# Optimization experiments

Hardware: AMD Instinct MI355X
Metric: run time of the kernel (lower is better)

The kernel has to match this reference:

```python
import jax, jax.numpy as jnp
import numpy as np

N, E, DIN, HID, DOUT = 50000, 800000, 128, 128, 64
NEG_SLOPE = 0.2


def setup_inputs() -> dict:
    key = jax.random.key(0)
    ks = jax.random.split(key, 16)
    x = jax.random.normal(ks[0], (N, DIN), dtype=jnp.float32)
    edge_index = jax.random.randint(ks[1], (2, E), 0, N, dtype=jnp.int64)

    def lin(k, fan_in, fan_out):
        kw, kb = jax.random.split(k)
        s = 1.0 / np.sqrt(fan_in)
        W = jax.random.uniform(kw, (fan_in, fan_out), jnp.float32, -s, s)
        b = jax.random.uniform(kb, (fan_out,), jnp.float32, -s, s)
        return W, b

    Wl, bl = lin(ks[2], DIN, DIN)   # GATv2 lin_l
    Wr, br = lin(ks[3], DIN, DIN)   # GATv2 lin_r
    att = jax.random.uniform(ks[4], (DIN,), jnp.float32, -1.0 / np.sqrt(DIN), 1.0 / np.sqrt(DIN))
    bg = jnp.zeros((DIN,), jnp.float32)  # GAT output bias
    W1, b1 = lin(ks[5], DIN, HID)   # ChebConv K=1 -> plain linear
    W2, b2 = lin(ks[6], HID, HID)
    W3, b3 = lin(ks[7], HID, DOUT)
    return {"x": x, "edge_index": edge_index, "Wl": Wl, "bl": bl, "Wr": Wr,
            "br": br, "att": att, "bg": bg, "W1": W1, "b1": b1,
            "W2": W2, "b2": b2, "W3": W3, "b3": b3}


def reference(x, edge_index, Wl, bl, Wr, br, att, bg, W1, b1, W2, b2, W3, b3):
    n = x.shape[0]
    # GATv2Conv adds self loops by default
    loop = jnp.arange(n, dtype=edge_index.dtype)
    src = jnp.concatenate([edge_index[0], loop])  # source j
    dst = jnp.concatenate([edge_index[1], loop])  # target i

    xl = x @ Wl + bl  # [N, DIN]
    xr = x @ Wr + br  # [N, DIN]

    # GATv2 edge scores: leaky_relu(x_l[j] + x_r[i]) . att
    e = jax.nn.leaky_relu(xl[src] + xr[dst], NEG_SLOPE)  # [E+N, DIN]
    a = e @ att                                          # [E+N]

    # softmax over incoming edges of each destination node
    amax = jax.ops.segment_max(a, dst, num_segments=n)
    ea = jnp.exp(a - amax[dst])
    denom = jax.ops.segment_sum(ea, dst, num_segments=n)
    alpha = ea / denom[dst]                              # [E+N]

    # aggregate messages alpha * x_l[j] at destinations
    h = jax.ops.segment_sum(alpha[:, None] * xl[src], dst, num_segments=n) + bg

    # ChebConv with K=1 reduces to a linear layer (T_0(L) = I)
    h = jax.nn.relu(h @ W1 + b1)
    h = jax.nn.relu(h @ W2 + b2)
    # dropout_rate = 0.0 -> identity
    return h @ W3 + b3
```

## Files before the change

### kernel.cpp

```cpp
#include <hip/hip_runtime.h>
#include <hip/hip_bf16.h>

#define DIN 128
#define NEG_SLOPE 0.2f
#define PTILE 1024
#define FCAP 8192
#define CVT_BLKS 289

typedef __attribute__((ext_vector_type(8))) short bf16x8;
typedef __attribute__((ext_vector_type(8))) unsigned short u16x8;
typedef __attribute__((ext_vector_type(4))) float f32x4;
typedef __attribute__((ext_vector_type(2))) float f32x2;
typedef __attribute__((ext_vector_type(4))) unsigned int u32x4;

__device__ __forceinline__ ushort f2bf(float f) {
  unsigned u = __float_as_uint(f);
  u += 0x7FFFu + ((u >> 16) & 1u);
  return (ushort)(u >> 16);
}
__device__ __forceinline__ f32x2 bfpair(unsigned u) {
  f32x2 r;
  r.x = __uint_as_float(u << 16);
  r.y = __uint_as_float(u & 0xFFFF0000u);
  return r;
}

template <int CTRL>
__device__ __forceinline__ float dppadd(float x) {
  int v = __builtin_amdgcn_update_dpp(0, __float_as_int(x), CTRL, 0xf, 0xf, true);
  return x + __int_as_float(v);
}
__device__ __forceinline__ float red16(float t) {
  t = dppadd<0xB1>(t);
  t = dppadd<0x4E>(t);
  t = dppadd<0x141>(t);
  t = dppadd<0x140>(t);
  return t;
}

__global__ __launch_bounds__(256) void cvt_hist_kernel(
    const float* __restrict__ Wl, const float* __restrict__ Wr,
    const float* __restrict__ W1, const float* __restrict__ W2,
    const float* __restrict__ W3,
    ushort* __restrict__ WlT, ushort* __restrict__ WrT,
    ushort* __restrict__ W1T, ushort* __restrict__ W2T,
    ushort* __restrict__ W3T,
    const int* __restrict__ ei, int* __restrict__ ghist, int E) {
  if (blockIdx.x < CVT_BLKS) {
    int i = blockIdx.x * 256 + threadIdx.x;
    if (i < 16384) {
      int k = i >> 7, c = i & 127; WlT[c * 128 + k] = f2bf(Wl[i]);
    } else if (i < 32768) {
      int j = i - 16384; int k = j >> 7, c = j & 127; WrT[c * 128 + k] = f2bf(Wr[j]);
    } else if (i < 49152) {
      int j = i - 32768; int k = j >> 7, c = j & 127; W1T[c * 128 + k] = f2bf(W1[j]);
    } else if (i < 65536) {
      int j = i - 49152; int k = j >> 7, c = j & 127; W2T[c * 128 + k] = f2bf(W2[j]);
    } else if (i < 73728) {
      int j = i - 65536; int k = j >> 6, c = j & 63; W3T[c * 128 + k] = f2bf(W3[j]);
    }
  } else {
    __shared__ int h[256];
    h[threadIdx.x] = 0;
    __syncthreads();
    int tile = blockIdx.x - CVT_BLKS;
    for (int e = tile * PTILE + threadIdx.x;
         e < min(E, (tile + 1) * PTILE); e += 256)
      atomicAdd(&h[ei[E + e] >> 8], 1);
    __syncthreads();
    if (h[threadIdx.x] > 0) atomicAdd(&ghist[threadIdx.x], h[threadIdx.x]);
  }
}

__global__ __launch_bounds__(256) void lin_partition_kernel(
    const float* __restrict__ x,
    const ushort* __restrict__ WlT, const float* __restrict__ bl,
    const ushort* __restrict__ WrT, const float* __restrict__ br,
    ushort* __restrict__ xl, ushort* __restrict__ xr, int n, int nblk_lin,
    const int* __restrict__ ei, unsigned* __restrict__ part,
    const int* __restrict__ ghist, int* __restrict__ cursor0, int E) {
  if ((int)blockIdx.x < nblk_lin) {
    const int tid = threadIdx.x;
    const int wv = tid >> 6, lane = tid & 63;
    const int m = lane & 15, quad = lane >> 4;
    const int colbase = (wv & 1) * 64;
    const int nodew = blockIdx.x * 32 + (wv >> 1) * 16;
    int arow = nodew + m; if (arow >= n) arow = n - 1;
    f32x4 accl[4], accr[4];
#pragma unroll
    for (int nt = 0; nt < 4; nt++) { accl[nt] = (f32x4){0,0,0,0}; accr[nt] = (f32x4){0,0,0,0}; }
#pragma unroll
    for (int kk = 0; kk < 4; kk++) {
      int k0 = kk * 32 + quad * 8;
      const float4* xp = (const float4*)(x + (long)arow * 128 + k0);
      float4 x0 = xp[0], x1 = xp[1];
      bf16x8 af;
      af[0] = (short)f2bf(x0.x); af[1] = (short)f2bf(x0.y);
      af[2] = (short)f2bf(x0.z); af[3] = (short)f2bf(x0.w);
      af[4] = (short)f2bf(x1.x); af[5] = (short)f2bf(x1.y);
      af[6] = (short)f2bf(x1.z); af[7] = (short)f2bf(x1.w);
#pragma unroll
      for (int nt = 0; nt < 4; nt++) {
        int brow = colbase + nt * 16 + m;
        bf16x8 bl8 = *(const bf16x8*)(WlT + brow * 128 + k0);
        bf16x8 br8 = *(const bf16x8*)(WrT + brow * 128 + k0);
        accl[nt] = __builtin_amdgcn_mfma_f32_16x16x32_bf16(af, bl8, accl[nt], 0, 0, 0);
        accr[nt] = __builtin_amdgcn_mfma_f32_16x16x32_bf16(af, br8, accr[nt], 0, 0, 0);
      }
    }
#pragma unroll
    for (int nt = 0; nt < 4; nt++) {
      int col = colbase + nt * 16 + m;
      float vbl = bl[col], vbr = br[col];
#pragma unroll
      for (int r = 0; r < 4; r++) {
        int node = nodew + quad * 4 + r;
        if (node < n) {
          xl[(long)node * 128 + col] = f2bf(accl[nt][r] + vbl);
          xr[(long)node * 128 + col] = f2bf(accr[nt][r] + vbr);
        }
      }
    }
  } else {
    __shared__ int hist[256], pref[256], sexcl[256], curs[256], gbase[256],
                   gsc[256];
    const int tid = threadIdx.x;
    const int gv0 = ghist[tid];
    gsc[tid] = gv0;
    hist[tid] = 0;
    __syncthreads();
    __shared__ unsigned buf[PTILE];
    const int tile0 = ((int)blockIdx.x - nblk_lin) * PTILE;
    const int tcount = min(PTILE, E - tile0);
    unsigned pk[PTILE / 256];
    int cnt = 0;
    for (int i = tid; i < tcount; i += 256) {
      int e = tile0 + i;
      int s = ei[e], d = ei[E + e];
      unsigned p = ((unsigned)d << 16) | (unsigned)s;
      pk[cnt++] = p;
      atomicAdd(&hist[d >> 8], 1);
    }
    __syncthreads();
    int v = hist[tid];
    pref[tid] = v;
    __syncthreads();
    for (int d = 1; d < 256; d <<= 1) {
      int t1 = (tid >= d) ? pref[tid - d] : 0;
      int t2 = (tid >= d) ? gsc[tid - d] : 0;
      __syncthreads();
      pref[tid] += t1;
      gsc[tid] += t2;
      __syncthreads();
    }
    int exc = pref[tid] - v;
    sexcl[tid] = exc;
    curs[tid] = exc;
    gbase[tid] = (gsc[tid] - gv0) + ((v > 0) ? atomicAdd(&cursor0[tid], v) : 0);
    __syncthreads();
    for (int j = 0; j < cnt; j++) {
      int b = pk[j] >> 24;
      int pos = atomicAdd(&curs[b], 1);
      buf[pos] = pk[j];
    }
    __syncthreads();
    for (int i = tid; i < tcount; i += 256) {
      unsigned p = buf[i];
      int b = p >> 24;
      part[gbase[b] + (i - sexcl[b])] = p;
    }
  }
}

__global__ __launch_bounds__(512) void fine_kernel(
    const unsigned* __restrict__ part, const int* __restrict__ ghist,
    int* __restrict__ offsets, ushort* __restrict__ ssrc,
    int N, int E, int nbuck) {
  __shared__ int hist[256], pref[256], curs[256], gsc[256];
  __shared__ unsigned buf[FCAP], buf2[FCAP];
  const int tid = threadIdx.x;
  const int b = blockIdx.x;
  if (tid < 256) {
    gsc[tid] = ghist[tid];
    hist[tid] = 0;
  }
  __syncthreads();
  for (int d = 1; d < 256; d <<= 1) {
    int t = (tid >= d && tid < 256) ? gsc[tid - d] : 0;
    __syncthreads();
    if (tid < 256) gsc[tid] += t;
    __syncthreads();
  }
  const int seg0 = (b == 0) ? 0 : gsc[b - 1];
  const int len = min(gsc[b] - seg0, FCAP);
  for (int i = tid; i < len; i += 512) {
    unsigned p = part[seg0 + i];
    buf[i] = p;
    atomicAdd(&hist[(p >> 16) & 255], 1);
  }
  __syncthreads();
  int v = (tid < 256) ? hist[tid] : 0;
  if (tid < 256) pref[tid] = v;
  __syncthreads();
  for (int d = 1; d < 256; d <<= 1) {
    int t = (tid >= d && tid < 256) ? pref[tid - d] : 0;
    __syncthreads();
    if (tid < 256) pref[tid] += t;
    __syncthreads();
  }
  if (tid < 256) {
    int exc = pref[tid] - v;
    curs[tid] = exc;
    int node = b * 256 + tid;
    if (node < N) offsets[node] = seg0 + exc;
  }
  if (b == nbuck - 1 && tid == 0) offsets[N] = E;
  __syncthreads();
  for (int i = tid; i < len; i += 512) {
    unsigned p = buf[i];
    int pos = atomicAdd(&curs[(p >> 16) & 255], 1);
    buf2[pos] = p;
  }
  __syncthreads();
  for (int i = tid; i < len; i += 512)
    ssrc[seg0 + i] = (ushort)(buf2[i] & 0xFFFFu);
}

#define LDSP 136
__global__ __launch_bounds__(256) void node_mlp_kernel(
    const ushort* __restrict__ xl, const ushort* __restrict__ xr,
    const float* __restrict__ att, const float* __restrict__ bg,
    const int* __restrict__ offsets, const ushort* __restrict__ ssrc,
    const ushort* __restrict__ W1T, const float* __restrict__ b1,
    const ushort* __restrict__ W2T, const float* __restrict__ b2,
    const ushort* __restrict__ W3T, const float* __restrict__ b3,
    float* __restrict__ out, int n) {
  __shared__ ushort hst[32][LDSP];
  __shared__ ushort act[32][LDSP];
  const int tid = threadIdx.x;
  const int wv = tid >> 6, lane = tid & 63;
  {
    const int eg = lane >> 4, sl = lane & 15;
    const ushort* __restrict__ xls = xl + sl * 8;
    f32x2 a06[4], a04[4], gvb[4];
    {
      const float4* ap = (const float4*)(att + sl * 8);
      float4 a0 = ap[0], a1 = ap[1];
      f32x2 av[4] = {{a0.x, a0.y}, {a0.z, a0.w}, {a1.x, a1.y}, {a1.z, a1.w}};
#pragma unroll
      for (int jp = 0; jp < 4; jp++) {
        a06[jp] = 0.6f * av[jp];
        a04[jp] = 0.4f * av[jp];
      }
      const float4* bp = (const float4*)(bg + sl * 8);
      float4 g0 = bp[0], g1 = bp[1];
      gvb[0] = (f32x2){g0.x, g0.y}; gvb[1] = (f32x2){g0.z, g0.w};
      gvb[2] = (f32x2){g1.x, g1.y}; gvb[3] = (f32x2){g1.z, g1.w};
    }
    for (int nn = 0; nn < 8; nn++) {
      const int node = (int)blockIdx.x * 32 + wv * 8 + nn;
      if (node >= n) continue;
      const int beg = offsets[node];
      const int end = offsets[node + 1];
      const int last = end - 1;
      int ia0 = beg + 2 * eg;
      int sa  = (int)ssrc[min(ia0, last)];
      int sb  = (int)ssrc[min(ia0 + 1, last)];
      int sa2 = (int)ssrc[min(ia0 + 8, last)];
      int sb2 = (int)ssrc[min(ia0 + 9, last)];
      u32x4 uva = *(const u32x4*)(xls + (long)sa * 128);
      u32x4 uvb = *(const u32x4*)(xls + (long)sb * 128);
      f32x2 r2[4], acc2[4];
      u32x4 rv = *(const u32x4*)(xr + (long)node * 128 + sl * 8);
      u32x4 lv = *(const u32x4*)(xls + (long)node * 128);
      float denom;
      {
        f32x2 t1 = {0.f, 0.f}, t2 = {0.f, 0.f};
        f32x2 l2[4];
#pragma unroll
        for (int jp = 0; jp < 4; jp++) {
          r2[jp] = bfpair(rv[jp]);
          l2[jp] = bfpair(lv[jp]);
          f32x2 v = l2[jp] + r2[jp];
          t1 += a06[jp] * v;
          t2 += a04[jp] * __builtin_elementwise_abs(v);
        }
        float t = red16(t1.x + t1.y + t2.x + t2.y);
        float es = __expf(t);
        denom = (eg == 0) ? es : 0.f;
#pragma unroll
        for (int jp = 0; jp < 4; jp++)
          acc2[jp] = (eg == 0) ? es * l2[jp] : (f32x2){0.f, 0.f};
      }
      for (int p = beg; p < end; p += 8) {
        u32x4 ca = uva, cb = uvb;
        int ia = p + 2 * eg;
        bool cva = ia < end, cvb = ia + 1 < end;
        uva = *(const u32x4*)(xls + (long)sa2 * 128);
        uvb = *(const u32x4*)(xls + (long)sb2 * 128);
        int ian = p + 16 + 2 * eg;
        sa2 = (int)ssrc[min(ian, last)];
        sb2 = (int)ssrc[min(ian + 1, last)];
        f32x2 ua2[4], ub2[4];
        f32x2 ta1 = {0.f, 0.f}, ta2 = {0.f, 0.f};
        f32x2 tb1 = {0.f, 0.f}, tb2 = {0.f, 0.f};
#pragma unroll
        for (int jp = 0; jp < 4; jp++) {
          ua2[jp] = bfpair(ca[jp]);
          ub2[jp] = bfpair(cb[jp]);
          f32x2 va2 = ua2[jp] + r2[jp];
          f32x2 vb2 = ub2[jp] + r2[jp];
          ta1 += a06[jp] * va2;
          ta2 += a04[jp] * __builtin_elementwise_abs(va2);
          tb1 += a06[jp] * vb2;
          tb2 += a04[jp] * __builtin_elementwise_abs(vb2);
        }
        float ta = red16(ta1.x + ta1.y + ta2.x + ta2.y);
        float tb = red16(tb1.x + tb1.y + tb2.x + tb2.y);
        float ea = cva ? __expf(ta) : 0.f;
        float eb = cvb ? __expf(tb) : 0.f;
        denom += ea + eb;
#pragma unroll
        for (int jp = 0; jp < 4; jp++)
          acc2[jp] += ea * ua2[jp] + eb * ub2[jp];
      }
#pragma unroll
      for (int jp = 0; jp < 4; jp++) {
        acc2[jp].x += __shfl_xor(acc2[jp].x, 16);
        acc2[jp].y += __shfl_xor(acc2[jp].y, 16);
        acc2[jp].x += __shfl_xor(acc2[jp].x, 32);
        acc2[jp].y += __shfl_xor(acc2[jp].y, 32);
      }
      denom += __shfl_xor(denom, 16);
      denom += __shfl_xor(denom, 32);
      if (eg == 0) {
        float inv = 1.0f / denom;
        u16x8 o;
#pragma unroll
        for (int jp = 0; jp < 4; jp++) {
          f32x2 hv = acc2[jp] * inv + gvb[jp];
          o[2 * jp]     = f2bf(hv.x);
          o[2 * jp + 1] = f2bf(hv.y);
        }
        *(u16x8*)(&hst[wv * 8 + nn][sl * 8]) = o;
      }
    }
  }
  __syncthreads();
  const int m = lane & 15, quad = lane >> 4;
  const int half = wv & 1, ng = wv >> 1;
  const int colbase = half * 64;
  const int nodew = (int)blockIdx.x * 32 + ng * 16;
  f32x4 acc[4];
#pragma unroll
  for (int nt = 0; nt < 4; nt++) acc[nt] = (f32x4){0,0,0,0};
#pragma unroll
  for (int kk = 0; kk < 4; kk++) {
    int k0 = kk * 32 + quad * 8;
    bf16x8 af = *(const bf16x8*)(&hst[ng * 16 + m][k0]);
#pragma unroll
    for (int nt = 0; nt < 4; nt++) {
      bf16x8 b8 = *(const bf16x8*)(W1T + (colbase + nt * 16 + m) * 128 + k0);
      acc[nt] = __builtin_amdgcn_mfma_f32_16x16x32_bf16(af, b8, acc[nt], 0, 0, 0);
    }
  }
#pragma unroll
  for (int nt = 0; nt < 4; nt++) {
    int col = colbase + nt * 16 + m;
    float b = b1[col];
#pragma unroll
    for (int r = 0; r < 4; r++)
      act[ng * 16 + quad * 4 + r][col] = f2bf(fmaxf(acc[nt][r] + b, 0.f));
  }
  __syncthreads();
#pragma unroll
  for (int nt = 0; nt < 4; nt++) acc[nt] = (f32x4){0,0,0,0};
#pragma unroll
  for (int kk = 0; kk < 4; kk++) {
    int k0 = kk * 32 + quad * 8;
    bf16x8 af = *(const bf16x8*)(&act[ng * 16 + m][k0]);
#pragma unroll
    for (int nt = 0; nt < 4; nt++) {
      bf16x8 b8 = *(const bf16x8*)(W2T + (colbase + nt * 16 + m) * 128 + k0);
      acc[nt] = __builtin_amdgcn_mfma_f32_16x16x32_bf16(af, b8, acc[nt], 0, 0, 0);
    }
  }
  __syncthreads();
#pragma unroll
  for (int nt = 0; nt < 4; nt++) {
    int col = colbase + nt * 16 + m;
    float b = b2[col];
#pragma unroll
    for (int r = 0; r < 4; r++)
      act[ng * 16 + quad * 4 + r][col] = f2bf(fmaxf(acc[nt][r] + b, 0.f));
  }
  __syncthreads();
  f32x4 acc3[2];
#pragma unroll
  for (int nt = 0; nt < 2; nt++) acc3[nt] = (f32x4){0,0,0,0};
#pragma unroll
  for (int kk = 0; kk < 4; kk++) {
    int k0 = kk * 32 + quad * 8;
    bf16x8 af = *(const bf16x8*)(&act[ng * 16 + m][k0]);
#pragma unroll
    for (int nt = 0; nt < 2; nt++) {
      bf16x8 b8 = *(const bf16x8*)(W3T + (half * 32 + nt * 16 + m) * 128 + k0);
      acc3[nt] = __builtin_amdgcn_mfma_f32_16x16x32_bf16(af, b8, acc3[nt], 0, 0, 0);
    }
  }
#pragma unroll
  for (int nt = 0; nt < 2; nt++) {
    int col = half * 32 + nt * 16 + m;
    float b = b3[col];
#pragma unroll
    for (int r = 0; r < 4; r++) {
      int node = nodew + quad * 4 + r;
      if (node < n) out[(long)node * 64 + col] = acc3[nt][r] + b;
    }
  }
}

extern "C" void kernel_launch(void* const* d_in, const int* in_sizes, int n_in,
                              void* d_out, int out_size, void* d_ws, size_t ws_size,
                              hipStream_t stream) {
  const float* x   = (const float*)d_in[0];
  const int*   ei  = (const int*)d_in[1];
  const float* Wl  = (const float*)d_in[2];
  const float* bl  = (const float*)d_in[3];
  const float* Wr  = (const float*)d_in[4];
  const float* br  = (const float*)d_in[5];
  const float* att = (const float*)d_in[6];
  const float* bg  = (const float*)d_in[7];
  const float* W1  = (const float*)d_in[8];
  const float* b1  = (const float*)d_in[9];
  const float* W2  = (const float*)d_in[10];
  const float* b2  = (const float*)d_in[11];
  const float* W3  = (const float*)d_in[12];
  const float* b3  = (const float*)d_in[13];
  float* out = (float*)d_out;

  const int N = in_sizes[0] / DIN;
  const int E = in_sizes[1] / 2;
  const int nbuck = (N + 255) >> 8;

  char* ws = (char*)d_ws;
  size_t off = 0;
  auto alloc = [&](size_t bytes) {
    void* p = ws + off;
    off += (bytes + 255) & ~(size_t)255;
    return p;
  };
  int* ghist     = (int*)alloc(256 * 4);
  int* cursor0   = (int*)alloc(256 * 4);
  int* offsets   = (int*)alloc(((size_t)N + 4) * 4);
  unsigned* part = (unsigned*)alloc((size_t)E * 4);
  ushort* ssrc   = (ushort*)alloc(((size_t)E + 16) * 2);
  ushort* xlb    = (ushort*)alloc((size_t)N * DIN * 2);
  ushort* xrb    = (ushort*)alloc((size_t)N * DIN * 2);
  ushort* WlT    = (ushort*)alloc(16384 * 2);
  ushort* WrT    = (ushort*)alloc(16384 * 2);
  ushort* W1T    = (ushort*)alloc(16384 * 2);
  ushort* W2T    = (ushort*)alloc(16384 * 2);
  ushort* W3T    = (ushort*)alloc(8192 * 2);
  (void)ws_size;

  hipMemsetAsync(ghist, 0, 512 * 4, stream);

  int ntile = (E + PTILE - 1) / PTILE;
  cvt_hist_kernel<<<CVT_BLKS + ntile, 256, 0, stream>>>(
      Wl, Wr, W1, W2, W3, WlT, WrT, W1T, W2T, W3T, ei, ghist, E);

  int nblk32 = (N + 31) / 32;
  lin_partition_kernel<<<nblk32 + ntile, 256, 0, stream>>>(
      x, WlT, bl, WrT, br, xlb, xrb, N, nblk32, ei, part, ghist, cursor0, E);

  fine_kernel<<<nbuck, 512, 0, stream>>>(part, ghist, offsets, ssrc, N, E, nbuck);

  node_mlp_kernel<<<nblk32, 256, 0, stream>>>(
      xlb, xrb, att, bg, offsets, ssrc,
      W1T, b1, W2T, b2, W3T, b3, out, N);
}
```

Before: 253.8 us.

## Split GAT aggregation from MLP and compute per-node degree histogram globally

The fused aggregation+MLP kernel, where each wave handled eight nodes in sequence, is split in two. A new aggregation kernel assigns one wave per node and writes h to a global bf16 buffer, and a separate MFMA kernel runs the three linear layers from that buffer. The fine sort kernel drops its LDS buffering and local histogram pass and instead uses a per-node in-degree histogram built with global atomics in the first kernel, scattering directly into ssrc. This aims to improve load balance and occupancy and removes the FCAP cap, at the cost of an extra launch, an h round trip through global memory, and 800k global atomics.

```diff
diff --git a/kernel.cpp b/kernel.cpp
--- a/kernel.cpp
+++ b/kernel.cpp
@@ -4,7 +4,6 @@
 #define DIN 128
 #define NEG_SLOPE 0.2f
 #define PTILE 1024
-#define FCAP 8192
 #define CVT_BLKS 289
 
 typedef __attribute__((ext_vector_type(8))) short bf16x8;
@@ -45,7 +44,8 @@
     ushort* __restrict__ WlT, ushort* __restrict__ WrT,
     ushort* __restrict__ W1T, ushort* __restrict__ W2T,
     ushort* __restrict__ W3T,
-    const int* __restrict__ ei, int* __restrict__ ghist, int E) {
+    const int* __restrict__ ei, int* __restrict__ ghist,
+    int* __restrict__ nhist, int E) {
   if (blockIdx.x < CVT_BLKS) {
     int i = blockIdx.x * 256 + threadIdx.x;
     if (i < 16384) {
@@ -65,8 +65,11 @@
     __syncthreads();
     int tile = blockIdx.x - CVT_BLKS;
     for (int e = tile * PTILE + threadIdx.x;
-         e < min(E, (tile + 1) * PTILE); e += 256)
-      atomicAdd(&h[ei[E + e] >> 8], 1);
+         e < min(E, (tile + 1) * PTILE); e += 256) {
+      int d = ei[E + e];
+      atomicAdd(&h[d >> 8], 1);
+      atomicAdd(&nhist[d], 1);
+    }
     __syncthreads();
     if (h[threadIdx.x] > 0) atomicAdd(&ghist[threadIdx.x], h[threadIdx.x]);
   }
@@ -174,190 +177,177 @@
 
 __global__ __launch_bounds__(512) void fine_kernel(
     const unsigned* __restrict__ part, const int* __restrict__ ghist,
+    const int* __restrict__ nhist,
     int* __restrict__ offsets, ushort* __restrict__ ssrc,
     int N, int E, int nbuck) {
-  __shared__ int hist[256], pref[256], curs[256], gsc[256];
-  __shared__ unsigned buf[FCAP], buf2[FCAP];
+  __shared__ int gsc[256], nsc[256], curs[256];
   const int tid = threadIdx.x;
   const int b = blockIdx.x;
+  int nv = 0;
   if (tid < 256) {
     gsc[tid] = ghist[tid];
-    hist[tid] = 0;
+    int node = b * 256 + tid;
+    nv = (node < N) ? nhist[node] : 0;
+    nsc[tid] = nv;
   }
   __syncthreads();
   for (int d = 1; d < 256; d <<= 1) {
-    int t = (tid >= d && tid < 256) ? gsc[tid - d] : 0;
-    __syncthreads();
-    if (tid < 256) gsc[tid] += t;
+    int t1 = (tid >= d && tid < 256) ? gsc[tid - d] : 0;
+    int t2 = (tid >= d && tid < 256) ? nsc[tid - d] : 0;
+    __syncthreads();
+    if (tid < 256) { gsc[tid] += t1; nsc[tid] += t2; }
     __syncthreads();
   }
   const int seg0 = (b == 0) ? 0 : gsc[b - 1];
-  const int len = min(gsc[b] - seg0, FCAP);
-  for (int i = tid; i < len; i += 512) {
-    unsigned p = part[seg0 + i];
-    buf[i] = p;
-    atomicAdd(&hist[(p >> 16) & 255], 1);
-  }
-  __syncthreads();
-  int v = (tid < 256) ? hist[tid] : 0;
-  if (tid < 256) pref[tid] = v;
-  __syncthreads();
-  for (int d = 1; d < 256; d <<= 1) {
-    int t = (tid >= d && tid < 256) ? pref[tid - d] : 0;
-    __syncthreads();
-    if (tid < 256) pref[tid] += t;
-    __syncthreads();
-  }
+  const int len = gsc[b] - seg0;
   if (tid < 256) {
-    int exc = pref[tid] - v;
-    curs[tid] = exc;
+    int o = seg0 + nsc[tid] - nv;
+    curs[tid] = o;
     int node = b * 256 + tid;
-    if (node < N) offsets[node] = seg0 + exc;
+    if (node < N) offsets[node] = o;
   }
   if (b == nbuck - 1 && tid == 0) offsets[N] = E;
   __syncthreads();
   for (int i = tid; i < len; i += 512) {
-    unsigned p = buf[i];
+    unsigned p = part[seg0 + i];
     int pos = atomicAdd(&curs[(p >> 16) & 255], 1);
-    buf2[pos] = p;
-  }
-  __syncthreads();
-  for (int i = tid; i < len; i += 512)
-    ssrc[seg0 + i] = (ushort)(buf2[i] & 0xFFFFu);
-}
-
-#define LDSP 136
-__global__ __launch_bounds__(256) void node_mlp_kernel(
+    ssrc[pos] = (ushort)(p & 0xFFFFu);
+  }
+}
+
+__global__ __launch_bounds__(256) void node_aggr_kernel(
     const ushort* __restrict__ xl, const ushort* __restrict__ xr,
     const float* __restrict__ att, const float* __restrict__ bg,
     const int* __restrict__ offsets, const ushort* __restrict__ ssrc,
+    ushort* __restrict__ h, int n) {
+  int wave = (int)((blockIdx.x * (long)blockDim.x + threadIdx.x) >> 6);
+  int lane = threadIdx.x & 63;
+  if (wave >= n) return;
+  const int node = wave;
+  const int eg = lane >> 4, sl = lane & 15;
+  const int beg = offsets[node];
+  const int end = offsets[node + 1];
+  const int last = end - 1;
+  const ushort* __restrict__ xls = xl + sl * 8;
+  int ia0 = beg + 2 * eg;
+  int sa  = (int)ssrc[min(ia0, last)];
+  int sb  = (int)ssrc[min(ia0 + 1, last)];
+  int sa2 = (int)ssrc[min(ia0 + 8, last)];
+  int sb2 = (int)ssrc[min(ia0 + 9, last)];
+  u32x4 uva = *(const u32x4*)(xls + (long)sa * 128);
+  u32x4 uvb = *(const u32x4*)(xls + (long)sb * 128);
+
+  f32x2 a06[4], a04[4], r2[4], acc2[4];
+  {
+    const float4* ap = (const float4*)(att + sl * 8);
+    float4 a0 = ap[0], a1 = ap[1];
+    f32x2 av[4] = {{a0.x, a0.y}, {a0.z, a0.w}, {a1.x, a1.y}, {a1.z, a1.w}};
+#pragma unroll
+    for (int jp = 0; jp < 4; jp++) {
+      a06[jp] = 0.6f * av[jp];
+      a04[jp] = 0.4f * av[jp];
+    }
+  }
+  u32x4 rv = *(const u32x4*)(xr + (long)node * 128 + sl * 8);
+  u32x4 lv = *(const u32x4*)(xls + (long)node * 128);
+  float denom;
+  {
+    f32x2 t1 = {0.f, 0.f}, t2 = {0.f, 0.f};
+    f32x2 l2[4];
+#pragma unroll
+    for (int jp = 0; jp < 4; jp++) {
+      r2[jp] = bfpair(rv[jp]);
+      l2[jp] = bfpair(lv[jp]);
+      f32x2 v = l2[jp] + r2[jp];
+      t1 += a06[jp] * v;
+      t2 += a04[jp] * __builtin_elementwise_abs(v);
+    }
+    float t = red16(t1.x + t1.y + t2.x + t2.y);
+    float es = __expf(t);
+    denom = (eg == 0) ? es : 0.f;
+#pragma unroll
+    for (int jp = 0; jp < 4; jp++)
+      acc2[jp] = (eg == 0) ? es * l2[jp] : (f32x2){0.f, 0.f};
+  }
+  for (int p = beg; p < end; p += 8) {
+    u32x4 ca = uva, cb = uvb;
+    int ia = p + 2 * eg;
+    bool cva = ia < end, cvb = ia + 1 < end;
+    uva = *(const u32x4*)(xls + (long)sa2 * 128);
+    uvb = *(const u32x4*)(xls + (long)sb2 * 128);
+    int ian = p + 16 + 2 * eg;
+    sa2 = (int)ssrc[min(ian, last)];
+    sb2 = (int)ssrc[min(ian + 1, last)];
+    f32x2 ua2[4], ub2[4];
+    f32x2 ta1 = {0.f, 0.f}, ta2 = {0.f, 0.f};
+    f32x2 tb1 = {0.f, 0.f}, tb2 = {0.f, 0.f};
+#pragma unroll
+    for (int jp = 0; jp < 4; jp++) {
+      ua2[jp] = bfpair(ca[jp]);
+      ub2[jp] = bfpair(cb[jp]);
+      f32x2 va2 = ua2[jp] + r2[jp];
+      f32x2 vb2 = ub2[jp] + r2[jp];
+      ta1 += a06[jp] * va2;
+      ta2 += a04[jp] * __builtin_elementwise_abs(va2);
+      tb1 += a06[jp] * vb2;
+      tb2 += a04[jp] * __builtin_elementwise_abs(vb2);
+    }
+    float ta = red16(ta1.x + ta1.y + ta2.x + ta2.y);
+    float tb = red16(tb1.x + tb1.y + tb2.x + tb2.y);
+    float ea = cva ? __expf(ta) : 0.f;
+    float eb = cvb ? __expf(tb) : 0.f;
+    denom += ea + eb;
+#pragma unroll
+    for (int jp = 0; jp < 4; jp++)
+      acc2[jp] += ea * ua2[jp] + eb * ub2[jp];
+  }
+#pragma unroll
+  for (int jp = 0; jp < 4; jp++) {
+    acc2[jp].x += __shfl_xor(acc2[jp].x, 16);
+    acc2[jp].y += __shfl_xor(acc2[jp].y, 16);
+    acc2[jp].x += __shfl_xor(acc2[jp].x, 32);
+    acc2[jp].y += __shfl_xor(acc2[jp].y, 32);
+  }
+  denom += __shfl_xor(denom, 16);
+  denom += __shfl_xor(denom, 32);
+  if (eg == 0) {
+    float inv = 1.0f / denom;
+    const float4* bp = (const float4*)(bg + sl * 8);
+    float4 g0 = bp[0], g1 = bp[1];
+    f32x2 gv[4] = {{g0.x, g0.y}, {g0.z, g0.w}, {g1.x, g1.y}, {g1.z, g1.w}};
+    u16x8 o;
+#pragma unroll
+    for (int jp = 0; jp < 4; jp++) {
+      f32x2 hv = acc2[jp] * inv + gv[jp];
+      o[2 * jp]     = f2bf(hv.x);
+      o[2 * jp + 1] = f2bf(hv.y);
+    }
+    *(u16x8*)(h + (long)node * 128 + sl * 8) = o;
+  }
+}
+
+#define LDSP 136
+__global__ __launch_bounds__(256) void mlp_mfma_kernel(
+    const ushort* __restrict__ hb,
     const ushort* __restrict__ W1T, const float* __restrict__ b1,
     const ushort* __restrict__ W2T, const float* __restrict__ b2,
     const ushort* __restrict__ W3T, const float* __restrict__ b3,
     float* __restrict__ out, int n) {
-  __shared__ ushort hst[32][LDSP];
   __shared__ ushort act[32][LDSP];
   const int tid = threadIdx.x;
   const int wv = tid >> 6, lane = tid & 63;
-  {
-    const int eg = lane >> 4, sl = lane & 15;
-    const ushort* __restrict__ xls = xl + sl * 8;
-    f32x2 a06[4], a04[4], gvb[4];
-    {
-      const float4* ap = (const float4*)(att + sl * 8);
-      float4 a0 = ap[0], a1 = ap[1];
-      f32x2 av[4] = {{a0.x, a0.y}, {a0.z, a0.w}, {a1.x, a1.y}, {a1.z, a1.w}};
-#pragma unroll
-      for (int jp = 0; jp < 4; jp++) {
-        a06[jp] = 0.6f * av[jp];
-        a04[jp] = 0.4f * av[jp];
-      }
-      const float4* bp = (const float4*)(bg + sl * 8);
-      float4 g0 = bp[0], g1 = bp[1];
-      gvb[0] = (f32x2){g0.x, g0.y}; gvb[1] = (f32x2){g0.z, g0.w};
-      gvb[2] = (f32x2){g1.x, g1.y}; gvb[3] = (f32x2){g1.z, g1.w};
-    }
-    for (int nn = 0; nn < 8; nn++) {
-      const int node = (int)blockIdx.x * 32 + wv * 8 + nn;
-      if (node >= n) continue;
-      const int beg = offsets[node];
-      const int end = offsets[node + 1];
-      const int last = end - 1;
-      int ia0 = beg + 2 * eg;
-      int sa  = (int)ssrc[min(ia0, last)];
-      int sb  = (int)ssrc[min(ia0 + 1, last)];
-      int sa2 = (int)ssrc[min(ia0 + 8, last)];
-      int sb2 = (int)ssrc[min(ia0 + 9, last)];
-      u32x4 uva = *(const u32x4*)(xls + (long)sa * 128);
-      u32x4 uvb = *(const u32x4*)(xls + (long)sb * 128);
-      f32x2 r2[4], acc2[4];
-      u32x4 rv = *(const u32x4*)(xr + (long)node * 128 + sl * 8);
-      u32x4 lv = *(const u32x4*)(xls + (long)node * 128);
-      float denom;
-      {
-        f32x2 t1 = {0.f, 0.f}, t2 = {0.f, 0.f};
-        f32x2 l2[4];
-#pragma unroll
-        for (int jp = 0; jp < 4; jp++) {
-          r2[jp] = bfpair(rv[jp]);
-          l2[jp] = bfpair(lv[jp]);
-          f32x2 v = l2[jp] + r2[jp];
-          t1 += a06[jp] * v;
-          t2 += a04[jp] * __builtin_elementwise_abs(v);
-        }
-        float t = red16(t1.x + t1.y + t2.x + t2.y);
-        float es = __expf(t);
-        denom = (eg == 0) ? es : 0.f;
-#pragma unroll
-        for (int jp = 0; jp < 4; jp++)
-          acc2[jp] = (eg == 0) ? es * l2[jp] : (f32x2){0.f, 0.f};
-      }
-      for (int p = beg; p < end; p += 8) {
-        u32x4 ca = uva, cb = uvb;
-        int ia = p + 2 * eg;
-        bool cva = ia < end, cvb = ia + 1 < end;
-        uva = *(const u32x4*)(xls + (long)sa2 * 128);
-        uvb = *(const u32x4*)(xls + (long)sb2 * 128);
-        int ian = p + 16 + 2 * eg;
-        sa2 = (int)ssrc[min(ian, last)];
-        sb2 = (int)ssrc[min(ian + 1, last)];
-        f32x2 ua2[4], ub2[4];
-        f32x2 ta1 = {0.f, 0.f}, ta2 = {0.f, 0.f};
-        f32x2 tb1 = {0.f, 0.f}, tb2 = {0.f, 0.f};
-#pragma unroll
-        for (int jp = 0; jp < 4; jp++) {
-          ua2[jp] = bfpair(ca[jp]);
-          ub2[jp] = bfpair(cb[jp]);
-          f32x2 va2 = ua2[jp] + r2[jp];
-          f32x2 vb2 = ub2[jp] + r2[jp];
-          ta1 += a06[jp] * va2;
-          ta2 += a04[jp] * __builtin_elementwise_abs(va2);
-          tb1 += a06[jp] * vb2;
-          tb2 += a04[jp] * __builtin_elementwise_abs(vb2);
-        }
-        float ta = red16(ta1.x + ta1.y + ta2.x + ta2.y);
-        float tb = red16(tb1.x + tb1.y + tb2.x + tb2.y);
-        float ea = cva ? __expf(ta) : 0.f;
-        float eb = cvb ? __expf(tb) : 0.f;
-        denom += ea + eb;
-#pragma unroll
-        for (int jp = 0; jp < 4; jp++)
-          acc2[jp] += ea * ua2[jp] + eb * ub2[jp];
-      }
-#pragma unroll
-      for (int jp = 0; jp < 4; jp++) {
-        acc2[jp].x += __shfl_xor(acc2[jp].x, 16);
-        acc2[jp].y += __shfl_xor(acc2[jp].y, 16);
-        acc2[jp].x += __shfl_xor(acc2[jp].x, 32);
-        acc2[jp].y += __shfl_xor(acc2[jp].y, 32);
-      }
-      denom += __shfl_xor(denom, 16);
-      denom += __shfl_xor(denom, 32);
-      if (eg == 0) {
-        float inv = 1.0f / denom;
-        u16x8 o;
-#pragma unroll
-        for (int jp = 0; jp < 4; jp++) {
-          f32x2 hv = acc2[jp] * inv + gvb[jp];
-          o[2 * jp]     = f2bf(hv.x);
-          o[2 * jp + 1] = f2bf(hv.y);
-        }
-        *(u16x8*)(&hst[wv * 8 + nn][sl * 8]) = o;
-      }
-    }
-  }
-  __syncthreads();
   const int m = lane & 15, quad = lane >> 4;
   const int half = wv & 1, ng = wv >> 1;
   const int colbase = half * 64;
-  const int nodew = (int)blockIdx.x * 32 + ng * 16;
+  const int nodew = blockIdx.x * 32 + ng * 16;
+  int arow = nodew + m; if (arow >= n) arow = n - 1;
   f32x4 acc[4];
 #pragma unroll
   for (int nt = 0; nt < 4; nt++) acc[nt] = (f32x4){0,0,0,0};
 #pragma unroll
   for (int kk = 0; kk < 4; kk++) {
     int k0 = kk * 32 + quad * 8;
-    bf16x8 af = *(const bf16x8*)(&hst[ng * 16 + m][k0]);
+    bf16x8 af = *(const bf16x8*)(hb + (long)arow * 128 + k0);
 #pragma unroll
     for (int nt = 0; nt < 4; nt++) {
       bf16x8 b8 = *(const bf16x8*)(W1T + (colbase + nt * 16 + m) * 128 + k0);
@@ -452,11 +442,13 @@
   };
   int* ghist     = (int*)alloc(256 * 4);
   int* cursor0   = (int*)alloc(256 * 4);
+  int* nhist     = (int*)alloc((size_t)N * 4);
   int* offsets   = (int*)alloc(((size_t)N + 4) * 4);
   unsigned* part = (unsigned*)alloc((size_t)E * 4);
   ushort* ssrc   = (ushort*)alloc(((size_t)E + 16) * 2);
   ushort* xlb    = (ushort*)alloc((size_t)N * DIN * 2);
   ushort* xrb    = (ushort*)alloc((size_t)N * DIN * 2);
+  ushort* hbf    = (ushort*)alloc((size_t)N * DIN * 2);
   ushort* WlT    = (ushort*)alloc(16384 * 2);
   ushort* WrT    = (ushort*)alloc(16384 * 2);
   ushort* W1T    = (ushort*)alloc(16384 * 2);
@@ -464,19 +456,23 @@
   ushort* W3T    = (ushort*)alloc(8192 * 2);
   (void)ws_size;
 
-  hipMemsetAsync(ghist, 0, 512 * 4, stream);
+  hipMemsetAsync(ghist, 0, 2048 + (size_t)N * 4, stream);
 
   int ntile = (E + PTILE - 1) / PTILE;
   cvt_hist_kernel<<<CVT_BLKS + ntile, 256, 0, stream>>>(
-      Wl, Wr, W1, W2, W3, WlT, WrT, W1T, W2T, W3T, ei, ghist, E);
+      Wl, Wr, W1, W2, W3, WlT, WrT, W1T, W2T, W3T, ei, ghist, nhist, E);
 
   int nblk32 = (N + 31) / 32;
   lin_partition_kernel<<<nblk32 + ntile, 256, 0, stream>>>(
       x, WlT, bl, WrT, br, xlb, xrb, N, nblk32, ei, part, ghist, cursor0, E);
 
-  fine_kernel<<<nbuck, 512, 0, stream>>>(part, ghist, offsets, ssrc, N, E, nbuck);
-
-  node_mlp_kernel<<<nblk32, 256, 0, stream>>>(
-      xlb, xrb, att, bg, offsets, ssrc,
-      W1T, b1, W2T, b2, W3T, b3, out, N);
-}
+  fine_kernel<<<nbuck, 512, 0, stream>>>(part, ghist, nhist, offsets, ssrc,
+                                         N, E, nbuck);
+
+  int nwblk = (N + 3) / 4;
+  node_aggr_kernel<<<nwblk, 256, 0, stream>>>(xlb, xrb, att, bg,
+                                              offsets, ssrc, hbf, N);
+
+  mlp_mfma_kernel<<<nblk32, 256, 0, stream>>>(hbf, W1T, b1, W2T, b2,
+                                              W3T, b3, out, N);
+}
```

After: 281.5 us. 1.11x slower.
